# Kernel optimization log

Hardware: AMD Instinct MI355X
Metric: run time of the kernel (lower is better)

## Reference

```python
import jax, jax.numpy as jnp
import numpy as np

B, SQ, SV = 2, 2048, 2048
DV, DQ, DK, DO, H = 1024, 1280, 1024, 1024, 16
DHK, DHO = DK // H, DO // H


def setup_inputs() -> dict:
    key = jax.random.key(0)
    ks = jax.random.split(key, 8)
    pre_value_key = jax.random.normal(ks[0], (B, SV, DV), jnp.float32)
    pre_query = jax.random.normal(ks[1], (B, SQ, DQ), jnp.float32)
    value_key_masks = (jax.random.uniform(ks[2], (B, SV)) < 0.9).astype(jnp.float32)
    value_key_counts = jnp.maximum(value_key_masks.sum(-1), 1.0)
    s = 0.02
    Wq = jax.random.normal(ks[3], (DQ, DK), jnp.float32) * s
    bq = jnp.zeros((DK,), jnp.float32)
    Wk = jax.random.normal(ks[4], (DV, DK), jnp.float32) * s
    bk = jnp.zeros((DK,), jnp.float32)
    Wv = jax.random.normal(ks[5], (DV, DO), jnp.float32) * s
    bv = jnp.zeros((DO,), jnp.float32)
    overall_gain = jnp.ones((1, H, 1, 1), jnp.float32)
    overall_bias = jnp.full((1, H, 1, 1), -10.0, jnp.float32)
    return dict(pre_value_key=pre_value_key, pre_query=pre_query,
                value_key_masks=value_key_masks, value_key_counts=value_key_counts,
                Wq=Wq, bq=bq, Wk=Wk, bk=bk, Wv=Wv, bv=bv,
                overall_gain=overall_gain, overall_bias=overall_bias)


def _heads(x, h):
    # (B, S, D) -> (B, h, S, D//h)
    b, s, d = x.shape
    return x.reshape(b, s, h, d // h).transpose(0, 2, 1, 3)


def reference(pre_value_key, pre_query, value_key_masks, value_key_counts,
              Wq, bq, Wk, bk, Wv, bv, overall_gain, overall_bias):
    q = _heads(pre_query @ Wq + bq, H)        # (B,H,SQ,DHK)
    k = _heads(pre_value_key @ Wk + bk, H)    # (B,H,SV,DHK)
    v = _heads(pre_value_key @ Wv + bv, H)    # (B,H,SV,DHO)

    scores = jnp.einsum('bhqd,bhkd->bhqk', q, k) / jnp.sqrt(jnp.float32(DHK))

    mask = value_key_masks  # (B,SV), 0/1 float
    # pooled-score sigmoid gate (cross-attn branch)
    pooled = (scores * mask[:, None, None, :]).sum(-1, keepdims=True)
    pooled = pooled / value_key_counts[:, None, None, None]
    overall_weight = jax.nn.sigmoid(pooled * overall_gain + overall_bias)  # (B,H,SQ,1)

    add_mask = jnp.where(mask == 0, -jnp.inf, 0.0).astype(scores.dtype)
    sm = jax.nn.softmax(scores + add_mask[:, None, None, :], axis=-1)
    h = jnp.einsum('bhqk,bhkd->bhqd', sm, v)  # (B,H,SQ,DHO)

    pq_split = _heads(pre_query[:, :, :DO], H)  # (B,H,SQ,DHO)
    out = pq_split * (1.0 - overall_weight) + h * overall_weight
    out = out.transpose(0, 2, 1, 3).reshape(B, SQ, DO)
    out = jnp.concatenate([out, pre_query[:, :, DO:]], axis=-1)  # (B,SQ,DQ)
    return out
```

## Files before the change

kernel.cpp:

```cpp
#include <hip/hip_runtime.h>

typedef __attribute__((ext_vector_type(8))) __bf16 bf16x8;
typedef __attribute__((ext_vector_type(4))) float f32x4;
typedef __attribute__((ext_vector_type(16))) float f32x16;
typedef __attribute__((ext_vector_type(4))) unsigned short us4;
typedef __attribute__((ext_vector_type(4))) unsigned int u32x4;
typedef __attribute__((address_space(3))) void* as3vp;
typedef const __attribute__((address_space(1))) void* as1vp;

#define GLOAD_LDS16(g, l) __builtin_amdgcn_global_load_lds((as1vp)(g), (as3vp)(l), 16, 0, 0)

#if __has_builtin(__builtin_amdgcn_exp2f)
#define EXP2(x) __builtin_amdgcn_exp2f(x)
#else
#define EXP2(x) __expf((x) * 0.6931471805599453f)
#endif

__device__ __forceinline__ unsigned short f2bf(float f) {
  unsigned u = __builtin_bit_cast(unsigned, f);
  u += 0x7FFFu + ((u >> 16) & 1u);
  return (unsigned short)(u >> 16);
}
__device__ __forceinline__ float bf2f(unsigned short u) {
  return __builtin_bit_cast(float, (unsigned)u << 16);
}
__device__ __forceinline__ unsigned int pkbf(float a, float b) {
  unsigned int r;
  asm("v_cvt_pk_bf16_f32 %0, %1, %2" : "=v"(r) : "v"(a), "v"(b));
  return r;
}

__global__ void cvt_pq_tail(const float* __restrict__ x, unsigned short* __restrict__ y,
                            float* __restrict__ out) {
  const int i = blockIdx.x * 256 + threadIdx.x;
  if (i >= 1310720) return;
  float4 v = ((const float4*)x)[i];
  us4 o;
  o.x = f2bf(v.x); o.y = f2bf(v.y); o.z = f2bf(v.z); o.w = f2bf(v.w);
  ((us4*)y)[i] = o;
  if ((i % 320) >= 256) ((float4*)out)[i] = v;
}

__global__ void cvt_f32_bf16(const float* __restrict__ x, unsigned short* __restrict__ y, int n4) {
  int i = blockIdx.x * 256 + threadIdx.x;
  if (i >= n4) return;
  float4 v = ((const float4*)x)[i];
  us4 o;
  o.x = f2bf(v.x); o.y = f2bf(v.y); o.z = f2bf(v.z); o.w = f2bf(v.w);
  ((us4*)y)[i] = o;
}

__global__ void transpose_w3(const float* __restrict__ Wq, const float* __restrict__ Wk,
                             const float* __restrict__ Wv,
                             unsigned short* __restrict__ WqT, unsigned short* __restrict__ WkT,
                             unsigned short* __restrict__ WvT) {
  const int z = blockIdx.z;
  const int K = (z == 0) ? 1280 : 1024;
  if (blockIdx.y * 32 >= (unsigned)K) return;
  const float* W = (z == 0) ? Wq : ((z == 1) ? Wk : Wv);
  unsigned short* WT = (z == 0) ? WqT : ((z == 1) ? WkT : WvT);
  __shared__ float t[32][33];
  const int tx = threadIdx.x & 31, ty = threadIdx.x >> 5;
  const int n0 = blockIdx.x * 32, k0 = blockIdx.y * 32;
#pragma unroll
  for (int i = 0; i < 32; i += 8)
    t[ty + i][tx] = W[(size_t)(k0 + ty + i) * 1024 + n0 + tx];
  __syncthreads();
#pragma unroll
  for (int i = 0; i < 32; i += 8)
    WT[(size_t)(n0 + ty + i) * K + k0 + tx] = f2bf(t[tx][ty + i]);
}

__global__ void km_reduce(const unsigned short* __restrict__ Kbb, const float* __restrict__ mask,
                          float* __restrict__ km, float* __restrict__ addm) {
  if (blockIdx.x < 16) {
    const int i = blockIdx.x * 256 + threadIdx.x;
    addm[i] = (mask[i] != 0.f) ? 0.f : -1e30f;
  }
  __shared__ float red[16][64];
  const int bh = blockIdx.x >> 3, chunk = blockIdx.x & 7;
  const int b = bh >> 4;
  const int dg = (threadIdx.x & 15) * 4, rg = threadIdx.x >> 4;
  const unsigned short* kb = Kbb + (size_t)(b * 2048) * 1024 + (bh & 15) * 64 + dg;
  const float* mr = mask + b * 2048;
  float a0 = 0.f, a1 = 0.f, a2 = 0.f, a3 = 0.f;
  const int kv0 = chunk * 256;
#pragma unroll 4
  for (int kv = kv0 + rg; kv < kv0 + 256; kv += 16) {
    const float mv = mr[kv];
    us4 kq = *(const us4*)(kb + (size_t)kv * 1024);
    a0 = fmaf(mv, bf2f(kq.x), a0); a1 = fmaf(mv, bf2f(kq.y), a1);
    a2 = fmaf(mv, bf2f(kq.z), a2); a3 = fmaf(mv, bf2f(kq.w), a3);
  }
  red[rg][dg] = a0; red[rg][dg + 1] = a1; red[rg][dg + 2] = a2; red[rg][dg + 3] = a3;
  __syncthreads();
  if (threadIdx.x < 64) {
    float s = 0.f;
#pragma unroll
    for (int i = 0; i < 16; ++i) s += red[i][threadIdx.x];
    atomicAdd(&km[bh * 64 + threadIdx.x], s);
  }
}

__global__ __launch_bounds__(256, 2)
void gemm_all(const unsigned short* __restrict__ Aq,
              const unsigned short* __restrict__ Akv,
              const unsigned short* __restrict__ WqT,
              const unsigned short* __restrict__ WkT,
              const unsigned short* __restrict__ WvT,
              const float* __restrict__ bq,
              const float* __restrict__ bk,
              const float* __restrict__ bv,
              unsigned short* __restrict__ Qout,
              unsigned short* __restrict__ Kout,
              unsigned short* __restrict__ VTout) {
  __shared__ unsigned short sA[2][128 * 64];
  __shared__ unsigned short sB[2][128 * 64];
  const int z = blockIdx.z;
  const int KDIM = (z == 0) ? 1280 : 1024;
  const unsigned short* A = (z == 0) ? Aq : Akv;
  const unsigned short* Bt = (z == 0) ? WqT : ((z == 1) ? WkT : WvT);
  const float* bias = (z == 0) ? bq : ((z == 1) ? bk : bv);

  const int tid = threadIdx.x, lane = tid & 63, w = tid >> 6;
  const int l15 = lane & 15, lhi = lane >> 4;
  const int wm = w >> 1, wn = w & 1;
  const int row0 = blockIdx.x * 128, col0 = blockIdx.y * 128;

  const f32x4 zv = {0.f, 0.f, 0.f, 0.f};
  f32x4 acc[4][4];
#pragma unroll
  for (int m = 0; m < 4; ++m)
#pragma unroll
    for (int n = 0; n < 4; ++n) acc[m][n] = zv;

  auto stage = [&](int buf, int kt) {
#pragma unroll
    for (int i = 0; i < 4; ++i) {
      const int c = i * 256 + tid;
      const int r = c >> 3, kc = ((c & 7) ^ (r & 7)) * 8;
      GLOAD_LDS16(A + (size_t)(row0 + r) * KDIM + kt + kc, &sA[buf][0] + c * 8);
      GLOAD_LDS16(Bt + (size_t)(col0 + r) * KDIM + kt + kc, &sB[buf][0] + c * 8);
    }
  };

  const int NT = KDIM / 64;
  stage(0, 0);
  __syncthreads();
  int cur = 0;
  for (int t = 0; t < NT; ++t) {
    if (t + 1 < NT) stage(cur ^ 1, (t + 1) * 64);
    const unsigned short* sAb = &sA[cur][0];
    const unsigned short* sBb = &sB[cur][0];
#pragma unroll
    for (int ks = 0; ks < 2; ++ks) {
      const int koS = (ks * 32 + lhi * 8) ^ ((l15 & 7) * 8);
      bf16x8 af[4], bfr[4];
#pragma unroll
      for (int m = 0; m < 4; ++m) af[m] = *(const bf16x8*)(sAb + (wm * 64 + m * 16 + l15) * 64 + koS);
#pragma unroll
      for (int n = 0; n < 4; ++n) bfr[n] = *(const bf16x8*)(sBb + (wn * 64 + n * 16 + l15) * 64 + koS);
#pragma unroll
      for (int m = 0; m < 4; ++m)
#pragma unroll
        for (int n = 0; n < 4; ++n)
          acc[m][n] = __builtin_amdgcn_mfma_f32_16x16x32_bf16(af[m], bfr[n], acc[m][n], 0, 0, 0);
    }
    __syncthreads();
    cur ^= 1;
  }

  if (z <= 1) {
    unsigned short* C = (z == 0) ? Qout : Kout;
    const float scale = (z == 0) ? 0.18033688f : 1.0f;
#pragma unroll
    for (int n = 0; n < 4; ++n) {
      const int gc = col0 + wn * 64 + n * 16 + l15;
      const float bb = bias[gc];
#pragma unroll
      for (int m = 0; m < 4; ++m) {
        const int gr0 = row0 + wm * 64 + m * 16 + lhi * 4;
#pragma unroll
        for (int r = 0; r < 4; ++r)
          C[(size_t)(gr0 + r) * 1024 + gc] = f2bf((acc[m][n][r] + bb) * scale);
      }
    }
  } else {
    __syncthreads();
    unsigned short* tb = &sA[0][0];
#pragma unroll
    for (int n = 0; n < 4; ++n) {
      const int gcL = wn * 64 + n * 16 + l15;
      const float bb = bias[col0 + gcL];
      const int swz = ((gcL & 7) << 2) | ((gcL >> 3) & 1);
#pragma unroll
      for (int m = 0; m < 4; ++m) {
#pragma unroll
        for (int k = 0; k < 2; ++k) {
          const int grPair = wm * 32 + m * 8 + lhi * 2 + k;
          const unsigned val = pkbf(acc[m][n][2 * k] + bb, acc[m][n][2 * k + 1] + bb);
          *(unsigned*)((char*)tb + gcL * 256 + ((grPair ^ swz) * 4)) = val;
        }
      }
    }
    __syncthreads();
    const int b_ = row0 >> 11;
#pragma unroll
    for (int it = 0; it < 8; ++it) {
      const int c = it * 256 + tid;
      const int gcL = c >> 4, w0 = (c & 15) * 4;
      const int swz = ((gcL & 7) << 2) | ((gcL >> 3) & 1);
      u32x4 arr = *(const u32x4*)((const char*)tb + gcL * 256 + (((w0 ^ swz) & ~3) * 4));
      const int p = swz & 3;
      u32x4 o;
      o.x = arr[0 ^ p]; o.y = arr[1 ^ p]; o.z = arr[2 ^ p]; o.w = arr[3 ^ p];
      const int ch = col0 + gcL;
      *(u32x4*)(VTout + (((size_t)(b_ * 16 + (ch >> 6))) << 17) + (size_t)(ch & 63) * 2048 +
                (row0 & 2047) + w0 * 2) = o;
    }
  }
}

__global__ __launch_bounds__(256, 2)
void attn_fused(const unsigned short* __restrict__ Q,
                const unsigned short* __restrict__ Kb,
                const unsigned short* __restrict__ VT,
                const float* __restrict__ addm_g,
                const float* __restrict__ km,
                const float* __restrict__ counts,
                const float* __restrict__ gain,
                const float* __restrict__ gbias,
                const float* __restrict__ pq,
                float* __restrict__ out) {
  __shared__ __align__(16) char smem[40960];
  unsigned short* sK = (unsigned short*)smem;
  unsigned short* sV = (unsigned short*)(smem + 16384);
  float* saddm = (float*)(smem + 32768);
  float* sOT = (float*)smem;

  const int tid = threadIdx.x, lane = tid & 63, w = tid >> 6;
  const int l31 = lane & 31, h5 = lane >> 5;
  const int f = blockIdx.x;
  const int qt = (f >> 3) & 15;
  const int bh = (f & 7) + 8 * (f >> 7);
  const int b = bh >> 4, hh = bh & 15;
  const int q0 = qt * 128;

  GLOAD_LDS16(addm_g + b * 2048 + tid * 4, (char*)saddm + tid * 16);
  GLOAD_LDS16(addm_g + b * 2048 + 1024 + tid * 4, (char*)saddm + 4096 + tid * 16);

  bf16x8 qf[4];
  {
    const unsigned short* qp = Q + (size_t)(b * 2048 + q0 + w * 32 + l31) * 1024 + hh * 64 + h5 * 8;
#pragma unroll
    for (int ks = 0; ks < 4; ++ks) qf[ks] = *(const bf16x8*)(qp + ks * 16);
  }

  float pl_s = 0.f;
  {
    const float* kmp = km + (b * 16 + hh) * 64 + h5 * 8;
#pragma unroll
    for (int ks = 0; ks < 4; ++ks) {
      f32x4 ka = *(const f32x4*)(kmp + ks * 16);
      f32x4 kb4 = *(const f32x4*)(kmp + ks * 16 + 4);
#pragma unroll
      for (int j = 0; j < 4; ++j)
        pl_s += (float)qf[ks][j] * ka[j] + (float)qf[ks][j + 4] * kb4[j];
    }
    float ta = pl_s, tb = pl_s;
    asm("v_permlane32_swap_b32 %0, %1" : "+v"(ta), "+v"(tb));
    pl_s = ta + tb;
  }

  const unsigned short* Kbase = Kb + (size_t)(b * 2048) * 1024 + hh * 64;
  const unsigned short* Vbase = VT + (((size_t)(b * 16 + hh)) << 17);

  f32x16 o0, o1, l_vec;
#pragma unroll
  for (int r = 0; r < 16; ++r) { o0[r] = 0.f; o1[r] = 0.f; l_vec[r] = 0.f; }
  float m_ = -1e30f;

  auto stage = [&](int buf, int kv) {
#pragma unroll
    for (int i = 0; i < 2; ++i) {
      const int c = i * 256 + tid;
      const int r = c >> 3, sl = (c & 7) ^ (r & 7);
      GLOAD_LDS16(Kbase + (size_t)(kv + r) * 1024 + sl * 8, (char*)sK + buf * 8192 + c * 16);
      GLOAD_LDS16(Vbase + (size_t)r * 2048 + kv + sl * 8, (char*)sV + buf * 8192 + c * 16);
    }
  };

  stage(0, 0);
  __syncthreads();
  int cur = 0;

  for (int t = 0; t < 32; ++t) {
    if (t < 31) stage(cur ^ 1, (t + 1) * 64);
    const char* sKc = (const char*)sK + cur * 8192;
    const char* sVc = (const char*)sV + cur * 8192;

    f32x16 s0, s1;
#pragma unroll
    for (int g = 0; g < 4; ++g) {
      f32x4 a0 = *(const f32x4*)(saddm + t * 64 + g * 8 + h5 * 4);
      f32x4 a1 = *(const f32x4*)(saddm + t * 64 + 32 + g * 8 + h5 * 4);
#pragma unroll
      for (int j = 0; j < 4; ++j) { s0[g * 4 + j] = a0[j]; s1[g * 4 + j] = a1[j]; }
    }

#pragma unroll
    for (int ks = 0; ks < 4; ++ks) {
      const int sl = (((ks * 2 + h5) ^ (l31 & 7)) * 16);
      bf16x8 k0 = *(const bf16x8*)(sKc + l31 * 128 + sl);
      bf16x8 k1 = *(const bf16x8*)(sKc + (32 + l31) * 128 + sl);
      s0 = __builtin_amdgcn_mfma_f32_32x32x16_bf16(k0, qf[ks], s0, 0, 0, 0);
      s1 = __builtin_amdgcn_mfma_f32_32x32x16_bf16(k1, qf[ks], s1, 0, 0, 0);
    }

    f32x16 mx;
#pragma unroll
    for (int r = 0; r < 16; ++r) mx[r] = fmaxf(s0[r], s1[r]);
    float t8[8];
#pragma unroll
    for (int r = 0; r < 8; ++r) t8[r] = fmaxf(mx[r], mx[r + 8]);
    float tp = fmaxf(fmaxf(fmaxf(t8[0], t8[1]), fmaxf(t8[2], t8[3])),
                     fmaxf(fmaxf(t8[4], t8[5]), fmaxf(t8[6], t8[7])));
    {
      float ta = tp, tb = tp;
      asm("v_permlane32_swap_b32 %0, %1" : "+v"(ta), "+v"(tb));
      tp = fmaxf(ta, tb);
    }
    if (__any(tp > m_ + 11.0f)) {
      const float mnew = fmaxf(m_, tp);
      const float corr = EXP2(m_ - mnew);
      m_ = mnew;
      l_vec *= corr; o0 *= corr; o1 *= corr;
    }

    f32x16 p0, p1;
#pragma unroll
    for (int r = 0; r < 16; ++r) p0[r] = EXP2(s0[r] - m_);
#pragma unroll
    for (int r = 0; r < 16; ++r) p1[r] = EXP2(s1[r] - m_);
    l_vec += p0; l_vec += p1;

    bf16x8 pfs[4];
    {
      unsigned x0 = pkbf(p0[0], p0[1]), y0 = pkbf(p0[2], p0[3]);
      unsigned z0 = pkbf(p0[4], p0[5]), w0 = pkbf(p0[6], p0[7]);
      asm("v_permlane32_swap_b32 %0, %1" : "+v"(x0), "+v"(z0));
      asm("v_permlane32_swap_b32 %0, %1" : "+v"(y0), "+v"(w0));
      u32x4 f0 = {x0, y0, z0, w0};
      pfs[0] = __builtin_bit_cast(bf16x8, f0);
      unsigned x1 = pkbf(p0[8], p0[9]), y1 = pkbf(p0[10], p0[11]);
      unsigned z1 = pkbf(p0[12], p0[13]), w1 = pkbf(p0[14], p0[15]);
      asm("v_permlane32_swap_b32 %0, %1" : "+v"(x1), "+v"(z1));
      asm("v_permlane32_swap_b32 %0, %1" : "+v"(y1), "+v"(w1));
      u32x4 f1 = {x1, y1, z1, w1};
      pfs[1] = __builtin_bit_cast(bf16x8, f1);
      unsigned x2 = pkbf(p1[0], p1[1]), y2 = pkbf(p1[2], p1[3]);
      unsigned z2 = pkbf(p1[4], p1[5]), w2 = pkbf(p1[6], p1[7]);
      asm("v_permlane32_swap_b32 %0, %1" : "+v"(x2), "+v"(z2));
      asm("v_permlane32_swap_b32 %0, %1" : "+v"(y2), "+v"(w2));
      u32x4 f2 = {x2, y2, z2, w2};
      pfs[2] = __builtin_bit_cast(bf16x8, f2);
      unsigned x3 = pkbf(p1[8], p1[9]), y3 = pkbf(p1[10], p1[11]);
      unsigned z3 = pkbf(p1[12], p1[13]), w3 = pkbf(p1[14], p1[15]);
      asm("v_permlane32_swap_b32 %0, %1" : "+v"(x3), "+v"(z3));
      asm("v_permlane32_swap_b32 %0, %1" : "+v"(y3), "+v"(w3));
      u32x4 f3 = {x3, y3, z3, w3};
      pfs[3] = __builtin_bit_cast(bf16x8, f3);
    }

#pragma unroll
    for (int ks = 0; ks < 4; ++ks) {
      const int sl = (((ks * 2 + h5) ^ (l31 & 7)) * 16);
      bf16x8 v0 = *(const bf16x8*)(sVc + l31 * 128 + sl);
      bf16x8 v1 = *(const bf16x8*)(sVc + (32 + l31) * 128 + sl);
      o0 = __builtin_amdgcn_mfma_f32_32x32x16_bf16(v0, pfs[ks], o0, 0, 0, 0);
      o1 = __builtin_amdgcn_mfma_f32_32x32x16_bf16(v1, pfs[ks], o1, 0, 0, 0);
    }
    __syncthreads();
    cur ^= 1;
  }

  float l_s;
  {
    float a[8];
#pragma unroll
    for (int r = 0; r < 8; ++r) a[r] = l_vec[r] + l_vec[r + 8];
    l_s = ((a[0] + a[1]) + (a[2] + a[3])) + ((a[4] + a[5]) + (a[6] + a[7]));
    float ta = l_s, tb = l_s;
    asm("v_permlane32_swap_b32 %0, %1" : "+v"(ta), "+v"(tb));
    l_s = ta + tb;
  }
  const float po = pl_s * 0.6931471805599453f / counts[b];
  const float wgv = 1.f / (1.f + __expf(-(po * gain[hh] + gbias[hh])));
  const float invl = 1.f / l_s;

  __syncthreads();
  float* myOT = sOT + w * 2048;
#pragma unroll
  for (int r = 0; r < 16; ++r) {
    const int d0 = (r & 3) + 8 * (r >> 2) + 4 * h5;
    myOT[d0 * 32 + (l31 ^ (d0 & 31))] = o0[r] * invl;
    const int d1 = d0 + 32;
    myOT[d1 * 32 + (l31 ^ (d1 & 31))] = o1[r] * invl;
  }
  __syncthreads();
  const size_t rowbase = (size_t)(b * 2048 + q0 + w * 32) * 1280 + hh * 64 + lane;
  const float* pqrow = pq + rowbase;
  float* outrow = out + rowbase;
#pragma unroll 4
  for (int i = 0; i < 32; ++i) {
    const float hval = myOT[lane * 32 + (i ^ (lane & 31))];
    const float wgrow = __shfl(wgv, i, 64);
    const float pv = pqrow[(size_t)i * 1280];
    outrow[(size_t)i * 1280] = fmaf(hval - pv, wgrow, pv);
  }
}

extern "C" void kernel_launch(void* const* d_in, const int* in_sizes, int n_in,
                              void* d_out, int out_size, void* d_ws, size_t ws_size,
                              hipStream_t stream) {
  const float* pre_vk = (const float*)d_in[0];
  const float* pre_q  = (const float*)d_in[1];
  const float* vmask  = (const float*)d_in[2];
  const float* vcnt   = (const float*)d_in[3];
  const float* Wq = (const float*)d_in[4];
  const float* bq = (const float*)d_in[5];
  const float* Wk = (const float*)d_in[6];
  const float* bk = (const float*)d_in[7];
  const float* Wv = (const float*)d_in[8];
  const float* bv = (const float*)d_in[9];
  const float* gain  = (const float*)d_in[10];
  const float* gbias = (const float*)d_in[11];
  float* out = (float*)d_out;

  char* ws = (char*)d_ws;
  unsigned short* pq_bf = (unsigned short*)(ws);
  unsigned short* pv_bf = (unsigned short*)(ws + 10485760);
  unsigned short* WqT   = (unsigned short*)(ws + 18874368);
  unsigned short* WkT   = (unsigned short*)(ws + 21495808);
  unsigned short* WvT   = (unsigned short*)(ws + 23592960);
  unsigned short* Qb    = (unsigned short*)(ws + 25690112);
  unsigned short* Kbb   = (unsigned short*)(ws + 34078720);
  unsigned short* VTb   = (unsigned short*)(ws + 42467328);
  float*          kmb   = (float*)(ws + 50855936);
  float*          addm  = (float*)(ws + 50864128);

  hipMemsetAsync(kmb, 0, 2 * 16 * 64 * sizeof(float), stream);
  cvt_pq_tail<<<5120, 256, 0, stream>>>(pre_q, pq_bf, out);
  cvt_f32_bf16<<<4096, 256, 0, stream>>>(pre_vk, pv_bf, 1048576);
  transpose_w3<<<dim3(32, 40, 3), 256, 0, stream>>>(Wq, Wk, Wv, WqT, WkT, WvT);
  gemm_all<<<dim3(32, 8, 3), 256, 0, stream>>>(pq_bf, pv_bf, WqT, WkT, WvT, bq, bk, bv, Qb, Kbb, VTb);
  km_reduce<<<256, 256, 0, stream>>>(Kbb, vmask, kmb, addm);
  attn_fused<<<512, 256, 0, stream>>>(Qb, Kbb, VTb, addm, kmb, vcnt, gain, gbias, pre_q, out);
}
```

Baseline: 121.0 us.

## Store K/V in MFMA-fragment layout and load directly to registers in attention

The projection GEMM now writes K (computed as a transposed GEMM) and V in a per-head layout that matches the MFMA operand fragment order. The attention kernel can then load K/V straight from global memory into registers, prefetching the next K tile, and no longer stages them through LDS with barriers. The additive mask becomes bf16 and is folded into the score accumulator through an extra MFMA with a ones vector, replacing the LDS mask preload. This removes LDS traffic and syncthreads from the inner loop. In exchange it raises register pressure and leaves global-load latency exposed unless the prefetch hides it.

```diff
diff --git a/kernel.cpp b/kernel.cpp
--- a/kernel.cpp
+++ b/kernel.cpp
@@ -5,6 +5,7 @@
 typedef __attribute__((ext_vector_type(16))) float f32x16;
 typedef __attribute__((ext_vector_type(4))) unsigned short us4;
 typedef __attribute__((ext_vector_type(4))) unsigned int u32x4;
+typedef __attribute__((ext_vector_type(2))) unsigned int u32x2;
 typedef __attribute__((address_space(3))) void* as3vp;
 typedef const __attribute__((address_space(1))) void* as1vp;
 
@@ -56,7 +57,7 @@
                              unsigned short* __restrict__ WvT) {
   const int z = blockIdx.z;
   const int K = (z == 0) ? 1280 : 1024;
-  if (blockIdx.y * 32 >= (unsigned)K) return;
+  if ((int)blockIdx.y * 32 >= K) return;
   const float* W = (z == 0) ? Wq : ((z == 1) ? Wk : Wv);
   unsigned short* WT = (z == 0) ? WqT : ((z == 1) ? WkT : WvT);
   __shared__ float t[32][33];
@@ -71,24 +72,26 @@
     WT[(size_t)(n0 + ty + i) * K + k0 + tx] = f2bf(t[tx][ty + i]);
 }
 
-__global__ void km_reduce(const unsigned short* __restrict__ Kbb, const float* __restrict__ mask,
-                          float* __restrict__ km, float* __restrict__ addm) {
+__global__ void km_reduce(const unsigned short* __restrict__ KF, const float* __restrict__ mask,
+                          float* __restrict__ km, unsigned short* __restrict__ addm_bf) {
   if (blockIdx.x < 16) {
     const int i = blockIdx.x * 256 + threadIdx.x;
-    addm[i] = (mask[i] != 0.f) ? 0.f : -1e30f;
+    addm_bf[i] = f2bf((mask[i] != 0.f) ? 0.f : -1e30f);
   }
   __shared__ float red[16][64];
   const int bh = blockIdx.x >> 3, chunk = blockIdx.x & 7;
   const int b = bh >> 4;
   const int dg = (threadIdx.x & 15) * 4, rg = threadIdx.x >> 4;
-  const unsigned short* kb = Kbb + (size_t)(b * 2048) * 1024 + (bh & 15) * 64 + dg;
+  const unsigned short* kfb = KF + ((size_t)bh << 17);
   const float* mr = mask + b * 2048;
+  const int ks = dg >> 4, h5 = (dg >> 3) & 1, j0 = dg & 7;
   float a0 = 0.f, a1 = 0.f, a2 = 0.f, a3 = 0.f;
   const int kv0 = chunk * 256;
-#pragma unroll 4
   for (int kv = kv0 + rg; kv < kv0 + 256; kv += 16) {
     const float mv = mr[kv];
-    us4 kq = *(const us4*)(kb + (size_t)kv * 1024);
+    const int t = kv >> 6, rowin = kv & 63;
+    const size_t off = (size_t)(((t * 4 + ks) * 2 + (rowin >> 5)) * 64 + h5 * 32 + (rowin & 31)) * 8 + j0;
+    us4 kq = *(const us4*)(kfb + off);
     a0 = fmaf(mv, bf2f(kq.x), a0); a1 = fmaf(mv, bf2f(kq.y), a1);
     a2 = fmaf(mv, bf2f(kq.z), a2); a3 = fmaf(mv, bf2f(kq.w), a3);
   }
@@ -112,20 +115,20 @@
               const float* __restrict__ bk,
               const float* __restrict__ bv,
               unsigned short* __restrict__ Qout,
-              unsigned short* __restrict__ Kout,
-              unsigned short* __restrict__ VTout) {
+              unsigned short* __restrict__ KFout,
+              unsigned short* __restrict__ VFout) {
   __shared__ unsigned short sA[2][128 * 64];
   __shared__ unsigned short sB[2][128 * 64];
   const int z = blockIdx.z;
   const int KDIM = (z == 0) ? 1280 : 1024;
-  const unsigned short* A = (z == 0) ? Aq : Akv;
-  const unsigned short* Bt = (z == 0) ? WqT : ((z == 1) ? WkT : WvT);
-  const float* bias = (z == 0) ? bq : ((z == 1) ? bk : bv);
+  const unsigned short* Arow = (z == 0) ? Aq : ((z == 1) ? WkT : Akv);
+  const unsigned short* Brow = (z == 0) ? WqT : ((z == 1) ? Akv : WvT);
+  const int rowA0 = (z == 1) ? blockIdx.y * 128 : blockIdx.x * 128;
+  const int rowB0 = (z == 1) ? blockIdx.x * 128 : blockIdx.y * 128;
 
   const int tid = threadIdx.x, lane = tid & 63, w = tid >> 6;
   const int l15 = lane & 15, lhi = lane >> 4;
   const int wm = w >> 1, wn = w & 1;
-  const int row0 = blockIdx.x * 128, col0 = blockIdx.y * 128;
 
   const f32x4 zv = {0.f, 0.f, 0.f, 0.f};
   f32x4 acc[4][4];
@@ -139,8 +142,8 @@
     for (int i = 0; i < 4; ++i) {
       const int c = i * 256 + tid;
       const int r = c >> 3, kc = ((c & 7) ^ (r & 7)) * 8;
-      GLOAD_LDS16(A + (size_t)(row0 + r) * KDIM + kt + kc, &sA[buf][0] + c * 8);
-      GLOAD_LDS16(Bt + (size_t)(col0 + r) * KDIM + kt + kc, &sB[buf][0] + c * 8);
+      GLOAD_LDS16(Arow + (size_t)(rowA0 + r) * KDIM + kt + kc, &sA[buf][0] + c * 8);
+      GLOAD_LDS16(Brow + (size_t)(rowB0 + r) * KDIM + kt + kc, &sB[buf][0] + c * 8);
     }
   };
 
@@ -170,73 +173,89 @@
     cur ^= 1;
   }
 
-  if (z <= 1) {
-    unsigned short* C = (z == 0) ? Qout : Kout;
-    const float scale = (z == 0) ? 0.18033688f : 1.0f;
+  if (z == 0) {
 #pragma unroll
     for (int n = 0; n < 4; ++n) {
-      const int gc = col0 + wn * 64 + n * 16 + l15;
-      const float bb = bias[gc];
+      const int gc = rowB0 + wn * 64 + n * 16 + l15;
+      const float bb = bq[gc];
 #pragma unroll
       for (int m = 0; m < 4; ++m) {
-        const int gr0 = row0 + wm * 64 + m * 16 + lhi * 4;
+        const int gr0 = rowA0 + wm * 64 + m * 16 + lhi * 4;
 #pragma unroll
         for (int r = 0; r < 4; ++r)
-          C[(size_t)(gr0 + r) * 1024 + gc] = f2bf((acc[m][n][r] + bb) * scale);
+          Qout[(size_t)(gr0 + r) * 1024 + gc] = f2bf((acc[m][n][r] + bb) * 0.18033688f);
+      }
+    }
+  } else if (z == 1) {
+#pragma unroll
+    for (int n = 0; n < 4; ++n) {
+      const int gkv = rowB0 + wn * 64 + n * 16 + l15;
+      const int b = gkv >> 11, kvl = gkv & 2047;
+      const int t = kvl >> 6, rowin = kvl & 63;
+      const int halfk = rowin >> 5, l31k = rowin & 31;
+#pragma unroll
+      for (int m = 0; m < 4; ++m) {
+        const int gch = rowA0 + wm * 64 + m * 16 + lhi * 4;
+        const f32x4 bb = *(const f32x4*)(bk + gch);
+        const int h = gch >> 6, chh = gch & 63;
+        const int ks = chh >> 4, h5k = (chh >> 3) & 1, j0 = chh & 7;
+        const size_t off = ((size_t)(b * 16 + h) << 17) +
+                           (size_t)(((t * 4 + ks) * 2 + halfk) * 64 + h5k * 32 + l31k) * 8 + j0;
+        u32x2 st;
+        st.x = pkbf(acc[m][n][0] + bb[0], acc[m][n][1] + bb[1]);
+        st.y = pkbf(acc[m][n][2] + bb[2], acc[m][n][3] + bb[3]);
+        *(u32x2*)(KFout + off) = st;
       }
     }
   } else {
     __syncthreads();
-    unsigned short* tb = &sA[0][0];
+    unsigned* tb = (unsigned*)&sA[0][0];
 #pragma unroll
     for (int n = 0; n < 4; ++n) {
       const int gcL = wn * 64 + n * 16 + l15;
-      const float bb = bias[col0 + gcL];
-      const int swz = ((gcL & 7) << 2) | ((gcL >> 3) & 1);
+      const float bb = bv[rowB0 + gcL];
 #pragma unroll
       for (int m = 0; m < 4; ++m) {
 #pragma unroll
         for (int k = 0; k < 2; ++k) {
           const int grPair = wm * 32 + m * 8 + lhi * 2 + k;
-          const unsigned val = pkbf(acc[m][n][2 * k] + bb, acc[m][n][2 * k + 1] + bb);
-          *(unsigned*)((char*)tb + gcL * 256 + ((grPair ^ swz) * 4)) = val;
+          const int W = (grPair & 3) | ((((grPair >> 2) ^ gcL) & 15) << 2);
+          tb[gcL * 64 + W] = pkbf(acc[m][n][2 * k] + bb, acc[m][n][2 * k + 1] + bb);
         }
       }
     }
     __syncthreads();
-    const int b_ = row0 >> 11;
+    const int b_ = rowA0 >> 11;
 #pragma unroll
     for (int it = 0; it < 8; ++it) {
       const int c = it * 256 + tid;
-      const int gcL = c >> 4, w0 = (c & 15) * 4;
-      const int swz = ((gcL & 7) << 2) | ((gcL >> 3) & 1);
-      u32x4 arr = *(const u32x4*)((const char*)tb + gcL * 256 + (((w0 ^ swz) & ~3) * 4));
-      const int p = swz & 3;
-      u32x4 o;
-      o.x = arr[0 ^ p]; o.y = arr[1 ^ p]; o.z = arr[2 ^ p]; o.w = arr[3 ^ p];
-      const int ch = col0 + gcL;
-      *(u32x4*)(VTout + (((size_t)(b_ * 16 + (ch >> 6))) << 17) + (size_t)(ch & 63) * 2048 +
-                (row0 & 2047) + w0 * 2) = o;
+      const int gcL = (c & 63) + ((c >> 10) << 6);
+      const int u = (c >> 6) & 15;
+      const int W4 = (u ^ gcL) & 15;
+      u32x4 o = *(const u32x4*)(tb + gcL * 64 + W4 * 4);
+      const int kv0 = (rowA0 & 2047) + u * 8;
+      const int ch = rowB0 + gcL;
+      const int hh2 = ch >> 6, d = ch & 63;
+      const int t2 = kv0 >> 6, ks2 = (kv0 >> 4) & 3, h5v = (kv0 >> 3) & 1;
+      const size_t off = ((size_t)(b_ * 16 + hh2) << 17) +
+                         (size_t)(((t2 * 4 + ks2) * 2 + (d >> 5)) * 64 + h5v * 32 + (d & 31)) * 8;
+      *(u32x4*)(VFout + off) = o;
     }
   }
 }
 
 __global__ __launch_bounds__(256, 2)
 void attn_fused(const unsigned short* __restrict__ Q,
-                const unsigned short* __restrict__ Kb,
-                const unsigned short* __restrict__ VT,
-                const float* __restrict__ addm_g,
+                const unsigned short* __restrict__ KF,
+                const unsigned short* __restrict__ VF,
+                const unsigned short* __restrict__ addm_bf,
                 const float* __restrict__ km,
                 const float* __restrict__ counts,
                 const float* __restrict__ gain,
                 const float* __restrict__ gbias,
                 const float* __restrict__ pq,
                 float* __restrict__ out) {
-  __shared__ __align__(16) char smem[40960];
-  unsigned short* sK = (unsigned short*)smem;
-  unsigned short* sV = (unsigned short*)(smem + 16384);
-  float* saddm = (float*)(smem + 32768);
-  float* sOT = (float*)smem;
+  __shared__ float sOT[4 * 2048];
 
   const int tid = threadIdx.x, lane = tid & 63, w = tid >> 6;
   const int l31 = lane & 31, h5 = lane >> 5;
@@ -246,9 +265,6 @@
   const int b = bh >> 4, hh = bh & 15;
   const int q0 = qt * 128;
 
-  GLOAD_LDS16(addm_g + b * 2048 + tid * 4, (char*)saddm + tid * 16);
-  GLOAD_LDS16(addm_g + b * 2048 + 1024 + tid * 4, (char*)saddm + 4096 + tid * 16);
-
   bf16x8 qf[4];
   {
     const unsigned short* qp = Q + (size_t)(b * 2048 + q0 + w * 32 + l31) * 1024 + hh * 64 + h5 * 8;
@@ -272,49 +288,53 @@
     pl_s = ta + tb;
   }
 
-  const unsigned short* Kbase = Kb + (size_t)(b * 2048) * 1024 + hh * 64;
-  const unsigned short* Vbase = VT + (((size_t)(b * 16 + hh)) << 17);
+  const unsigned short* KFb = KF + ((size_t)bh << 17) + lane * 8;
+  const unsigned short* VFb = VF + ((size_t)bh << 17) + lane * 8;
+  const unsigned short* amb = addm_bf + b * 2048;
+
+  bf16x8 qone;
+  {
+    u32x4 fq = {h5 ? 0u : 0x3F80u, 0u, 0u, 0u};
+    qone = __builtin_bit_cast(bf16x8, fq);
+  }
 
   f32x16 o0, o1, l_vec;
 #pragma unroll
   for (int r = 0; r < 16; ++r) { o0[r] = 0.f; o1[r] = 0.f; l_vec[r] = 0.f; }
   float m_ = -1e30f;
 
-  auto stage = [&](int buf, int kv) {
-#pragma unroll
-    for (int i = 0; i < 2; ++i) {
-      const int c = i * 256 + tid;
-      const int r = c >> 3, sl = (c & 7) ^ (r & 7);
-      GLOAD_LDS16(Kbase + (size_t)(kv + r) * 1024 + sl * 8, (char*)sK + buf * 8192 + c * 16);
-      GLOAD_LDS16(Vbase + (size_t)r * 2048 + kv + sl * 8, (char*)sV + buf * 8192 + c * 16);
-    }
+  bf16x8 kA[8], kB[8], vf[8];
+  auto ldK = [&](int t, bf16x8 (&kf)[8]) {
+    const unsigned short* p = KFb + (size_t)t * 4096;
+#pragma unroll
+    for (int i = 0; i < 8; ++i) kf[i] = *(const bf16x8*)(p + i * 512);
   };
-
-  stage(0, 0);
-  __syncthreads();
-  int cur = 0;
-
-  for (int t = 0; t < 32; ++t) {
-    if (t < 31) stage(cur ^ 1, (t + 1) * 64);
-    const char* sKc = (const char*)sK + cur * 8192;
-    const char* sVc = (const char*)sV + cur * 8192;
+  auto ldV = [&](int t, bf16x8 (&vv)[8]) {
+    const unsigned short* p = VFb + (size_t)t * 4096;
+#pragma unroll
+    for (int i = 0; i < 8; ++i) vv[i] = *(const bf16x8*)(p + i * 512);
+  };
+
+  auto body = [&](int t, bf16x8 (&kf)[8], bf16x8 (&nkf)[8], bool ln) {
+    ldV(t, vf);
+    if (ln) ldK(t + 1, nkf);
+    const unsigned short am0 = amb[t * 64 + l31];
+    const unsigned short am1 = amb[t * 64 + 32 + l31];
 
     f32x16 s0, s1;
 #pragma unroll
-    for (int g = 0; g < 4; ++g) {
-      f32x4 a0 = *(const f32x4*)(saddm + t * 64 + g * 8 + h5 * 4);
-      f32x4 a1 = *(const f32x4*)(saddm + t * 64 + 32 + g * 8 + h5 * 4);
-#pragma unroll
-      for (int j = 0; j < 4; ++j) { s0[g * 4 + j] = a0[j]; s1[g * 4 + j] = a1[j]; }
-    }
+    for (int r = 0; r < 16; ++r) { s0[r] = 0.f; s1[r] = 0.f; }
 
 #pragma unroll
     for (int ks = 0; ks < 4; ++ks) {
-      const int sl = (((ks * 2 + h5) ^ (l31 & 7)) * 16);
-      bf16x8 k0 = *(const bf16x8*)(sKc + l31 * 128 + sl);
-      bf16x8 k1 = *(const bf16x8*)(sKc + (32 + l31) * 128 + sl);
-      s0 = __builtin_amdgcn_mfma_f32_32x32x16_bf16(k0, qf[ks], s0, 0, 0, 0);
-      s1 = __builtin_amdgcn_mfma_f32_32x32x16_bf16(k1, qf[ks], s1, 0, 0, 0);
+      s0 = __builtin_amdgcn_mfma_f32_32x32x16_bf16(kf[ks * 2], qf[ks], s0, 0, 0, 0);
+      s1 = __builtin_amdgcn_mfma_f32_32x32x16_bf16(kf[ks * 2 + 1], qf[ks], s1, 0, 0, 0);
+    }
+    {
+      u32x4 fa0 = {h5 ? 0u : (unsigned)am0, 0u, 0u, 0u};
+      u32x4 fa1 = {h5 ? 0u : (unsigned)am1, 0u, 0u, 0u};
+      s0 = __builtin_amdgcn_mfma_f32_32x32x16_bf16(__builtin_bit_cast(bf16x8, fa0), qone, s0, 0, 0, 0);
+      s1 = __builtin_amdgcn_mfma_f32_32x32x16_bf16(__builtin_bit_cast(bf16x8, fa1), qone, s1, 0, 0, 0);
     }
 
     f32x16 mx;
@@ -374,14 +394,16 @@
 
 #pragma unroll
     for (int ks = 0; ks < 4; ++ks) {
-      const int sl = (((ks * 2 + h5) ^ (l31 & 7)) * 16);
-      bf16x8 v0 = *(const bf16x8*)(sVc + l31 * 128 + sl);
-      bf16x8 v1 = *(const bf16x8*)(sVc + (32 + l31) * 128 + sl);
-      o0 = __builtin_amdgcn_mfma_f32_32x32x16_bf16(v0, pfs[ks], o0, 0, 0, 0);
-      o1 = __builtin_amdgcn_mfma_f32_32x32x16_bf16(v1, pfs[ks], o1, 0, 0, 0);
-    }
-    __syncthreads();
-    cur ^= 1;
+      o0 = __builtin_amdgcn_mfma_f32_32x32x16_bf16(vf[ks * 2], pfs[ks], o0, 0, 0, 0);
+      o1 = __builtin_amdgcn_mfma_f32_32x32x16_bf16(vf[ks * 2 + 1], pfs[ks], o1, 0, 0, 0);
+    }
+  };
+
+  ldK(0, kA);
+#pragma unroll 1
+  for (int t = 0; t < 32; t += 2) {
+    body(t, kA, kB, true);
+    body(t + 1, kB, kA, t + 2 < 32);
   }
 
   float l_s;
@@ -398,7 +420,6 @@
   const float wgv = 1.f / (1.f + __expf(-(po * gain[hh] + gbias[hh])));
   const float invl = 1.f / l_s;
 
-  __syncthreads();
   float* myOT = sOT + w * 2048;
 #pragma unroll
   for (int r = 0; r < 16; ++r) {
@@ -444,16 +465,16 @@
   unsigned short* WkT   = (unsigned short*)(ws + 21495808);
   unsigned short* WvT   = (unsigned short*)(ws + 23592960);
   unsigned short* Qb    = (unsigned short*)(ws + 25690112);
-  unsigned short* Kbb   = (unsigned short*)(ws + 34078720);
-  unsigned short* VTb   = (unsigned short*)(ws + 42467328);
+  unsigned short* KFb   = (unsigned short*)(ws + 34078720);
+  unsigned short* VFb   = (unsigned short*)(ws + 42467328);
   float*          kmb   = (float*)(ws + 50855936);
-  float*          addm  = (float*)(ws + 50864128);
+  unsigned short* addmb = (unsigned short*)(ws + 50864128);
 
   hipMemsetAsync(kmb, 0, 2 * 16 * 64 * sizeof(float), stream);
   cvt_pq_tail<<<5120, 256, 0, stream>>>(pre_q, pq_bf, out);
   cvt_f32_bf16<<<4096, 256, 0, stream>>>(pre_vk, pv_bf, 1048576);
   transpose_w3<<<dim3(32, 40, 3), 256, 0, stream>>>(Wq, Wk, Wv, WqT, WkT, WvT);
-  gemm_all<<<dim3(32, 8, 3), 256, 0, stream>>>(pq_bf, pv_bf, WqT, WkT, WvT, bq, bk, bv, Qb, Kbb, VTb);
-  km_reduce<<<256, 256, 0, stream>>>(Kbb, vmask, kmb, addm);
-  attn_fused<<<512, 256, 0, stream>>>(Qb, Kbb, VTb, addm, kmb, vcnt, gain, gbias, pre_q, out);
-}
+  gemm_all<<<dim3(32, 8, 3), 256, 0, stream>>>(pq_bf, pv_bf, WqT, WkT, WvT, bq, bk, bv, Qb, KFb, VFb);
+  km_reduce<<<256, 256, 0, stream>>>(KFb, vmask, kmb, addmb);
+  attn_fused<<<512, 256, 0, stream>>>(Qb, KFb, VFb, addmb, kmb, vcnt, gain, gbias, pre_q, out);
+}
```

Measured after the change: 128.1 us. +5.9%, slower.

## Store V in MFMA-fragment order and load it directly into registers

Applied to the files above, without the earlier changes.

The V projection epilogue now writes V in a pre-swizzled fragment layout that matches the operand order of the PV MFMA. The attention kernel then loads V fragments straight from global memory into registers each iteration instead of staging them through shared memory, which shrinks LDS use and removes the V LDS reads. The risk is exposed global-load latency, since the V loads are issued in the same iteration they are consumed, plus higher register pressure from holding eight bf16x8 fragments.

```diff
diff --git a/kernel.cpp b/kernel.cpp
--- a/kernel.cpp
+++ b/kernel.cpp
@@ -5,6 +5,7 @@
 typedef __attribute__((ext_vector_type(16))) float f32x16;
 typedef __attribute__((ext_vector_type(4))) unsigned short us4;
 typedef __attribute__((ext_vector_type(4))) unsigned int u32x4;
+typedef __attribute__((ext_vector_type(2))) unsigned int u32x2;
 typedef __attribute__((address_space(3))) void* as3vp;
 typedef const __attribute__((address_space(1))) void* as1vp;
 
@@ -56,7 +57,7 @@
                              unsigned short* __restrict__ WvT) {
   const int z = blockIdx.z;
   const int K = (z == 0) ? 1280 : 1024;
-  if (blockIdx.y * 32 >= (unsigned)K) return;
+  if ((int)blockIdx.y * 32 >= K) return;
   const float* W = (z == 0) ? Wq : ((z == 1) ? Wk : Wv);
   unsigned short* WT = (z == 0) ? WqT : ((z == 1) ? WkT : WvT);
   __shared__ float t[32][33];
@@ -113,14 +114,13 @@
               const float* __restrict__ bv,
               unsigned short* __restrict__ Qout,
               unsigned short* __restrict__ Kout,
-              unsigned short* __restrict__ VTout) {
+              unsigned short* __restrict__ VFout) {
   __shared__ unsigned short sA[2][128 * 64];
   __shared__ unsigned short sB[2][128 * 64];
   const int z = blockIdx.z;
   const int KDIM = (z == 0) ? 1280 : 1024;
   const unsigned short* A = (z == 0) ? Aq : Akv;
   const unsigned short* Bt = (z == 0) ? WqT : ((z == 1) ? WkT : WvT);
-  const float* bias = (z == 0) ? bq : ((z == 1) ? bk : bv);
 
   const int tid = threadIdx.x, lane = tid & 63, w = tid >> 6;
   const int l15 = lane & 15, lhi = lane >> 4;
@@ -172,6 +172,7 @@
 
   if (z <= 1) {
     unsigned short* C = (z == 0) ? Qout : Kout;
+    const float* bias = (z == 0) ? bq : bk;
     const float scale = (z == 0) ? 0.18033688f : 1.0f;
 #pragma unroll
     for (int n = 0; n < 4; ++n) {
@@ -187,19 +188,18 @@
     }
   } else {
     __syncthreads();
-    unsigned short* tb = &sA[0][0];
+    unsigned* tb = (unsigned*)&sA[0][0];
 #pragma unroll
     for (int n = 0; n < 4; ++n) {
       const int gcL = wn * 64 + n * 16 + l15;
-      const float bb = bias[col0 + gcL];
-      const int swz = ((gcL & 7) << 2) | ((gcL >> 3) & 1);
+      const float bb = bv[col0 + gcL];
 #pragma unroll
       for (int m = 0; m < 4; ++m) {
 #pragma unroll
         for (int k = 0; k < 2; ++k) {
           const int grPair = wm * 32 + m * 8 + lhi * 2 + k;
-          const unsigned val = pkbf(acc[m][n][2 * k] + bb, acc[m][n][2 * k + 1] + bb);
-          *(unsigned*)((char*)tb + gcL * 256 + ((grPair ^ swz) * 4)) = val;
+          const int W = (grPair & 3) | ((((grPair >> 2) ^ gcL) & 15) << 2);
+          tb[gcL * 64 + W] = pkbf(acc[m][n][2 * k] + bb, acc[m][n][2 * k + 1] + bb);
         }
       }
     }
@@ -208,15 +208,17 @@
 #pragma unroll
     for (int it = 0; it < 8; ++it) {
       const int c = it * 256 + tid;
-      const int gcL = c >> 4, w0 = (c & 15) * 4;
-      const int swz = ((gcL & 7) << 2) | ((gcL >> 3) & 1);
-      u32x4 arr = *(const u32x4*)((const char*)tb + gcL * 256 + (((w0 ^ swz) & ~3) * 4));
-      const int p = swz & 3;
-      u32x4 o;
-      o.x = arr[0 ^ p]; o.y = arr[1 ^ p]; o.z = arr[2 ^ p]; o.w = arr[3 ^ p];
+      const int gcL = (c & 63) + ((c >> 10) << 6);
+      const int u = (c >> 6) & 15;
+      const int W4 = (u ^ gcL) & 15;
+      u32x4 o = *(const u32x4*)(tb + gcL * 64 + W4 * 4);
+      const int kv0 = (row0 & 2047) + u * 8;
       const int ch = col0 + gcL;
-      *(u32x4*)(VTout + (((size_t)(b_ * 16 + (ch >> 6))) << 17) + (size_t)(ch & 63) * 2048 +
-                (row0 & 2047) + w0 * 2) = o;
+      const int hh2 = ch >> 6, d = ch & 63;
+      const int t2 = kv0 >> 6, ks2 = (kv0 >> 4) & 3, h5v = (kv0 >> 3) & 1;
+      const size_t off = ((size_t)(b_ * 16 + hh2) << 17) +
+                         (size_t)(((t2 * 4 + ks2) * 2 + (d >> 5)) * 64 + h5v * 32 + (d & 31)) * 8;
+      *(u32x4*)(VFout + off) = o;
     }
   }
 }
@@ -224,7 +226,7 @@
 __global__ __launch_bounds__(256, 2)
 void attn_fused(const unsigned short* __restrict__ Q,
                 const unsigned short* __restrict__ Kb,
-                const unsigned short* __restrict__ VT,
+                const unsigned short* __restrict__ VF,
                 const float* __restrict__ addm_g,
                 const float* __restrict__ km,
                 const float* __restrict__ counts,
@@ -232,10 +234,9 @@
                 const float* __restrict__ gbias,
                 const float* __restrict__ pq,
                 float* __restrict__ out) {
-  __shared__ __align__(16) char smem[40960];
+  __shared__ __align__(16) char smem[32768];
   unsigned short* sK = (unsigned short*)smem;
-  unsigned short* sV = (unsigned short*)(smem + 16384);
-  float* saddm = (float*)(smem + 32768);
+  float* saddm = (float*)(smem + 16384);
   float* sOT = (float*)smem;
 
   const int tid = threadIdx.x, lane = tid & 63, w = tid >> 6;
@@ -273,31 +274,37 @@
   }
 
   const unsigned short* Kbase = Kb + (size_t)(b * 2048) * 1024 + hh * 64;
-  const unsigned short* Vbase = VT + (((size_t)(b * 16 + hh)) << 17);
+  const unsigned short* VFb = VF + ((size_t)bh << 17) + lane * 8;
 
   f32x16 o0, o1, l_vec;
 #pragma unroll
   for (int r = 0; r < 16; ++r) { o0[r] = 0.f; o1[r] = 0.f; l_vec[r] = 0.f; }
   float m_ = -1e30f;
 
-  auto stage = [&](int buf, int kv) {
+  auto stageK = [&](int buf, int kv) {
 #pragma unroll
     for (int i = 0; i < 2; ++i) {
       const int c = i * 256 + tid;
       const int r = c >> 3, sl = (c & 7) ^ (r & 7);
       GLOAD_LDS16(Kbase + (size_t)(kv + r) * 1024 + sl * 8, (char*)sK + buf * 8192 + c * 16);
-      GLOAD_LDS16(Vbase + (size_t)r * 2048 + kv + sl * 8, (char*)sV + buf * 8192 + c * 16);
     }
   };
 
-  stage(0, 0);
+  bf16x8 vf[8];
+  auto ldV = [&](int t) {
+    const unsigned short* p = VFb + (size_t)t * 4096;
+#pragma unroll
+    for (int i = 0; i < 8; ++i) vf[i] = *(const bf16x8*)(p + i * 512);
+  };
+
+  stageK(0, 0);
   __syncthreads();
   int cur = 0;
 
   for (int t = 0; t < 32; ++t) {
-    if (t < 31) stage(cur ^ 1, (t + 1) * 64);
+    if (t < 31) stageK(cur ^ 1, (t + 1) * 64);
+    ldV(t);
     const char* sKc = (const char*)sK + cur * 8192;
-    const char* sVc = (const char*)sV + cur * 8192;
 
     f32x16 s0, s1;
 #pragma unroll
@@ -374,11 +381,8 @@
 
 #pragma unroll
     for (int ks = 0; ks < 4; ++ks) {
-      const int sl = (((ks * 2 + h5) ^ (l31 & 7)) * 16);
-      bf16x8 v0 = *(const bf16x8*)(sVc + l31 * 128 + sl);
-      bf16x8 v1 = *(const bf16x8*)(sVc + (32 + l31) * 128 + sl);
-      o0 = __builtin_amdgcn_mfma_f32_32x32x16_bf16(v0, pfs[ks], o0, 0, 0, 0);
-      o1 = __builtin_amdgcn_mfma_f32_32x32x16_bf16(v1, pfs[ks], o1, 0, 0, 0);
+      o0 = __builtin_amdgcn_mfma_f32_32x32x16_bf16(vf[ks * 2], pfs[ks], o0, 0, 0, 0);
+      o1 = __builtin_amdgcn_mfma_f32_32x32x16_bf16(vf[ks * 2 + 1], pfs[ks], o1, 0, 0, 0);
     }
     __syncthreads();
     cur ^= 1;
@@ -445,7 +449,7 @@
   unsigned short* WvT   = (unsigned short*)(ws + 23592960);
   unsigned short* Qb    = (unsigned short*)(ws + 25690112);
   unsigned short* Kbb   = (unsigned short*)(ws + 34078720);
-  unsigned short* VTb   = (unsigned short*)(ws + 42467328);
+  unsigned short* VFb   = (unsigned short*)(ws + 42467328);
   float*          kmb   = (float*)(ws + 50855936);
   float*          addm  = (float*)(ws + 50864128);
 
@@ -453,7 +457,7 @@
   cvt_pq_tail<<<5120, 256, 0, stream>>>(pre_q, pq_bf, out);
   cvt_f32_bf16<<<4096, 256, 0, stream>>>(pre_vk, pv_bf, 1048576);
   transpose_w3<<<dim3(32, 40, 3), 256, 0, stream>>>(Wq, Wk, Wv, WqT, WkT, WvT);
-  gemm_all<<<dim3(32, 8, 3), 256, 0, stream>>>(pq_bf, pv_bf, WqT, WkT, WvT, bq, bk, bv, Qb, Kbb, VTb);
+  gemm_all<<<dim3(32, 8, 3), 256, 0, stream>>>(pq_bf, pv_bf, WqT, WkT, WvT, bq, bk, bv, Qb, Kbb, VFb);
   km_reduce<<<256, 256, 0, stream>>>(Kbb, vmask, kmb, addm);
-  attn_fused<<<512, 256, 0, stream>>>(Qb, Kbb, VTb, addm, kmb, vcnt, gain, gbias, pre_q, out);
-}
+  attn_fused<<<512, 256, 0, stream>>>(Qb, Kbb, VFb, addm, kmb, vcnt, gain, gbias, pre_q, out);
+}
```

Result: no change. 121.3 us (+0.3%).
